# Kernel tuning notes

Measured on AMD Instinct MI355X. Metric: run time of the kernel, lower is better.

## Reference

```python
import jax, jax.numpy as jnp
import numpy as np

EMBED = 1024
HEADS = 16
HEAD_DIM = EMBED // HEADS
OUT = 1024


def setup_inputs() -> dict:
    key = jax.random.key(0)
    ks = jax.random.split(key, 6)
    x = jax.random.normal(ks[0], (4, 2048, EMBED), dtype=jnp.float32)
    # per-head projection weights, torch Linear convention: [out_features, in_features]
    s = 1.0 / np.sqrt(HEAD_DIM)
    Wv = jax.random.uniform(ks[1], (HEAD_DIM, HEAD_DIM), jnp.float32, -s, s)
    Wk = jax.random.uniform(ks[2], (HEAD_DIM, HEAD_DIM), jnp.float32, -s, s)
    Wq = jax.random.uniform(ks[3], (HEAD_DIM, HEAD_DIM), jnp.float32, -s, s)
    so = 1.0 / np.sqrt(EMBED)
    Wo = jax.random.uniform(ks[4], (OUT, EMBED), jnp.float32, -so, so)
    bo = jax.random.uniform(ks[5], (OUT,), jnp.float32, -so, so)
    return {"x": x, "Wq": Wq, "Wk": Wk, "Wv": Wv, "Wo": Wo, "bo": bo}


def reference(x, Wq, Wk, Wv, Wo, bo):
    N, L, _ = x.shape
    xh = x.reshape(N, L, HEADS, HEAD_DIM)  # nqhd
    q = jnp.einsum('nqhd,ed->nqhe', xh, Wq)
    k = jnp.einsum('nkhd,ed->nkhe', xh, Wk)
    v = jnp.einsum('nkhd,ed->nkhe', xh, Wv)
    # full score matrix [N, H, Q, K], scaled by sqrt(embed_size) as in source
    energy = jnp.einsum('nqhd,nkhd->nhqk', q, k) / np.sqrt(EMBED).astype(np.float32)
    attn = jax.nn.softmax(energy, axis=3)
    out = jnp.einsum('nhqk,nkhd->nqhd', attn, v).reshape(N, L, EMBED)
    return out @ Wo.T + bo
```

## Files before the change

### kernel.cpp

```cpp
#include <hip/hip_runtime.h>
#include <hip/hip_bf16.h>
#include <stdint.h>
#include <stddef.h>


typedef __attribute__((ext_vector_type(8))) short bf16x8;
typedef __attribute__((ext_vector_type(4))) float f32x4;
typedef __attribute__((ext_vector_type(4))) short short4v;
typedef __attribute__((ext_vector_type(2))) uint32_t uint2v;

__device__ __forceinline__ f32x4 mfma16(bf16x8 a, bf16x8 b, f32x4 c) {
    return __builtin_amdgcn_mfma_f32_16x16x32_bf16(a, b, c, 0, 0, 0);
}

__device__ __forceinline__ short f2bf(float x) {
    union { float f; uint32_t u; } v; v.f = x;
    uint32_t r = (v.u + 0x7FFFu + ((v.u >> 16) & 1u)) >> 16;
    return (short)(uint16_t)r;
}

__device__ __forceinline__ uint32_t pk2bf(float a, float b) {
    union { __hip_bfloat162 h; uint32_t u; } v;
    v.h = __float22bfloat162_rn(float2{a, b});
    return v.u;
}

__device__ __forceinline__ bf16x8 cvt8(const float* __restrict__ p) {
    f32x4 a = *(const f32x4*)p;
    f32x4 b = *(const f32x4*)(p + 4);
    bf16x8 r;
    r[0] = f2bf(a[0]); r[1] = f2bf(a[1]); r[2] = f2bf(a[2]); r[3] = f2bf(a[3]);
    r[4] = f2bf(b[0]); r[5] = f2bf(b[1]); r[6] = f2bf(b[2]); r[7] = f2bf(b[3]);
    return r;
}

__device__ __forceinline__ void swap16(uint32_t a, uint32_t b,
                                       uint32_t& lo, uint32_t& hi) {
#if __has_builtin(__builtin_amdgcn_permlane16_swap)
    uint2v r = __builtin_amdgcn_permlane16_swap(a, b, false, false);
    lo = r[0]; hi = r[1];
#else
    int lane = (int)(threadIdx.x & 63);
    uint32_t bl = (uint32_t)__shfl((int)b, lane & 47);
    uint32_t ah = (uint32_t)__shfl((int)a, lane | 16);
    lo = (lane & 16) ? bl : a;
    hi = (lane & 16) ? b : ah;
#endif
}

__global__ __launch_bounds__(256)
void wpack_kernel(const float* __restrict__ Wo, const float* __restrict__ Wq,
                  const float* __restrict__ Wk, const float* __restrict__ Wv,
                  short* __restrict__ wo_f, short* __restrict__ wqkv_f) {
    int b = blockIdx.x;
    if (b < 512) {
        int idx = b * 256 + threadIdx.x;
        int nrow = idx >> 7;
        int k0 = (idx & 127) * 8;
        bf16x8 v = cvt8(Wo + (size_t)nrow * 1024 + k0);
        int ntile = nrow >> 4, lcn = nrow & 15;
        int kseg = k0 >> 5, qd = (k0 >> 3) & 3;
        *(bf16x8*)(wo_f + ((size_t)(ntile * 32 + kseg) * 64 + qd * 16 + lcn) * 8) = v;
    } else {
        const float* W = (b == 512) ? Wq : (b == 513) ? Wk : Wv;
        short* dst = wqkv_f + (size_t)(b - 512) * 4096;
        for (int u = threadIdx.x; u < 512; u += 256) {
            int seg = u >> 6, ln = u & 63;
            int nt = seg >> 1, kf = seg & 1, lq = ln >> 4, lcn = ln & 15;
            bf16x8 v = cvt8(W + (nt * 16 + lcn) * 64 + kf * 32 + lq * 8);
            *(bf16x8*)(dst + u * 8) = v;
        }
    }
}

__global__ __launch_bounds__(256)
void kvproj_kernel(const float* __restrict__ x, const short* __restrict__ wqkv_f,
                   short* __restrict__ kf_ws, short* __restrict__ vf_ws) {
    __shared__ alignas(16) short kbuf[128 * 72];
    __shared__ alignas(16) short vbuf[64 * 136];
    int tid = threadIdx.x;
    int lt = blockIdx.x & 15, nh = blockIdx.x >> 4;
    int n = nh >> 4, h = nh & 15;
    int l0 = lt * 128, kt0 = lt * 2;
    int wv = tid >> 6, lane = tid & 63, quad = lane >> 4, lc = lane & 15;
    const short* wkf = wqkv_f + 4096 + lane * 8;
    const short* wvf = wqkv_f + 8192 + lane * 8;

    for (int u = tid; u < 1024; u += 256) {
        int r = u >> 3, c = (u & 7) * 8;
        *(bf16x8*)(kbuf + r * 72 + c) =
            cvt8(x + (size_t)(n * 2048 + l0 + r) * 1024 + h * 64 + c);
    }
    __syncthreads();

    bf16x8 xa[2][2];
    for (int mt = 0; mt < 2; ++mt)
        for (int kf = 0; kf < 2; ++kf)
            xa[mt][kf] = *(bf16x8*)(kbuf + (wv * 32 + mt * 16 + lc) * 72 + kf * 32 + quad * 8);

    f32x4 ka[2][4] = {}, va[2][4] = {};
    for (int nt = 0; nt < 4; ++nt)
        for (int kf = 0; kf < 2; ++kf) {
            bf16x8 wkb = *(const bf16x8*)(wkf + (nt * 2 + kf) * 512);
            bf16x8 wvb = *(const bf16x8*)(wvf + (nt * 2 + kf) * 512);
            for (int mt = 0; mt < 2; ++mt) {
                ka[mt][nt] = mfma16(xa[mt][kf], wkb, ka[mt][nt]);
                va[mt][nt] = mfma16(xa[mt][kf], wvb, va[mt][nt]);
            }
        }

    for (int mt = 0; mt < 2; ++mt) {
        int off = wv * 32 + mt * 16;
        for (int nt = 0; nt < 4; ++nt) {
            short4v pv;
            for (int i = 0; i < 4; ++i) {
                kbuf[(off + quad * 4 + i) * 72 + nt * 16 + lc] = f2bf(ka[mt][nt][i]);
                pv[i] = f2bf(va[mt][nt][i]);
            }
            *(short4v*)(vbuf + (nt * 16 + lc) * 136 + off + quad * 4) = pv;
        }
    }
    __syncthreads();

    size_t base = (size_t)nh * 131072 + (size_t)kt0 * 4096;
    for (int u = tid; u < 1024; u += 256) {
        int tile = u >> 9, rem = u & 511, seg = rem >> 6, ln = u & 63;
        int t = seg >> 1, kf = seg & 1;
        int lq = ln >> 4, ll = ln & 15;
        int bq = ((lq & 1) << 1) | (lq >> 1);
        bf16x8 kw = *(bf16x8*)(kbuf + (tile * 64 + t * 16 + ll) * 72 + kf * 32 + lq * 8);
        *(bf16x8*)(kf_ws + base + (size_t)tile * 4096 + seg * 512 + ln * 8) = kw;
        bf16x8 vw = *(bf16x8*)(vbuf + (t * 16 + ll) * 136 + tile * 64 + kf * 32 + bq * 8);
        *(bf16x8*)(vf_ws + base + (size_t)tile * 4096 + seg * 512 + ln * 8) = vw;
    }
}

__global__ __launch_bounds__(256, 2)
void flash_kernel(const float* __restrict__ x, const short* __restrict__ wqkv_f,
                  const short* __restrict__ kf_ws, const short* __restrict__ vf_ws,
                  short* __restrict__ ao) {
    __shared__ alignas(16) short pbuf[128 * 72];
    int tid = threadIdx.x;
    int nh = blockIdx.x & 63, qt = blockIdx.x >> 6;
    int n = nh >> 4, h = nh & 15;
    int q0 = qt * 128;
    int wv = tid >> 6, lane = tid & 63, quad = lane >> 4, lc = lane & 15;

    for (int u = tid; u < 1024; u += 256) {
        int r = u >> 3, c = (u & 7) * 8;
        *(bf16x8*)(pbuf + r * 72 + c) =
            cvt8(x + (size_t)(n * 2048 + q0 + r) * 1024 + h * 64 + c);
    }
    __syncthreads();
    {
        const short* wqf = wqkv_f + lane * 8;
        bf16x8 xa[2][2];
        for (int mt = 0; mt < 2; ++mt)
            for (int kf = 0; kf < 2; ++kf)
                xa[mt][kf] = *(bf16x8*)(pbuf + (wv * 32 + mt * 16 + lc) * 72 +
                                        kf * 32 + quad * 8);
        f32x4 qacc[2][4] = {};
        for (int nt = 0; nt < 4; ++nt)
            for (int kf = 0; kf < 2; ++kf) {
                bf16x8 wb = *(const bf16x8*)(wqf + (nt * 2 + kf) * 512);
                for (int mt = 0; mt < 2; ++mt)
                    qacc[mt][nt] = mfma16(xa[mt][kf], wb, qacc[mt][nt]);
            }
        const float QS = 0.04508422002778011f;
        for (int mt = 0; mt < 2; ++mt)
            for (int nt = 0; nt < 4; ++nt)
                for (int i = 0; i < 4; ++i)
                    pbuf[(wv * 32 + mt * 16 + quad * 4 + i) * 72 + nt * 16 + lc] =
                        f2bf(qacc[mt][nt][i] * QS);
    }
    __syncthreads();
    bf16x8 qa[2][2];
    for (int mt = 0; mt < 2; ++mt)
        for (int kf = 0; kf < 2; ++kf)
            qa[mt][kf] = *(bf16x8*)(pbuf + (wv * 32 + mt * 16 + lc) * 72 +
                                    kf * 32 + quad * 8);

    f32x4 o[2][4] = {};
    float lsum[2] = {0.f, 0.f};
    const short* kbase = kf_ws + (size_t)nh * 131072 + lane * 8;
    const short* vbase = vf_ws + (size_t)nh * 131072 + lane * 8;

    bf16x8 kN[4][2];
    bf16x8 vA[4][2];
    f32x4 s[2][4];

#pragma unroll
    for (int t = 0; t < 4; ++t)
        for (int kf = 0; kf < 2; ++kf)
            kN[t][kf] = *(const bf16x8*)(kbase + (t * 2 + kf) * 512);
#pragma unroll
    for (int q2 = 0; q2 < 2; ++q2)
        for (int t = 0; t < 4; ++t) {
            f32x4 acc = {};
            acc = mfma16(kN[t][0], qa[q2][0], acc);
            acc = mfma16(kN[t][1], qa[q2][1], acc);
            s[q2][t] = acc;
        }

    for (int kt = 0; kt < 32; ++kt) {
        const short* vp = vbase + (size_t)kt * 4096;
        const short* kp = kbase + (size_t)((kt + 1) & 31) * 4096;
#pragma unroll
        for (int t = 0; t < 4; ++t)
            for (int kf = 0; kf < 2; ++kf)
                vA[t][kf] = *(const bf16x8*)(vp + (t * 2 + kf) * 512);
#pragma unroll
        for (int t = 0; t < 4; ++t)
            for (int kf = 0; kf < 2; ++kf)
                kN[t][kf] = *(const bf16x8*)(kp + (t * 2 + kf) * 512);

#pragma unroll
        for (int q2 = 0; q2 < 2; ++q2) {
            uint32_t p0[4], p1[4];
            float ts = 0.f;
#pragma unroll
            for (int t = 0; t < 4; ++t) {
                float e0 = __builtin_amdgcn_exp2f(s[q2][t][0]);
                float e1 = __builtin_amdgcn_exp2f(s[q2][t][1]);
                float e2 = __builtin_amdgcn_exp2f(s[q2][t][2]);
                float e3 = __builtin_amdgcn_exp2f(s[q2][t][3]);
                ts += (e0 + e1) + (e2 + e3);
                p0[t] = pk2bf(e0, e1);
                p1[t] = pk2bf(e2, e3);
            }
            lsum[q2] += ts;
#pragma unroll
            for (int kf = 0; kf < 2; ++kf) {
                uint32_t r0, r1, r2, r3;
                swap16(p0[2 * kf], p0[2 * kf + 1], r0, r2);
                swap16(p1[2 * kf], p1[2 * kf + 1], r1, r3);
                union { uint32_t u[4]; bf16x8 v; } fr;
                fr.u[0] = r0; fr.u[1] = r1; fr.u[2] = r2; fr.u[3] = r3;
#pragma unroll
                for (int dt = 0; dt < 4; ++dt)
                    o[q2][dt] = mfma16(vA[dt][kf], fr.v, o[q2][dt]);
            }
        }

#pragma unroll
        for (int q2 = 0; q2 < 2; ++q2)
            for (int t = 0; t < 4; ++t) {
                f32x4 acc = {};
                acc = mfma16(kN[t][0], qa[q2][0], acc);
                acc = mfma16(kN[t][1], qa[q2][1], acc);
                s[q2][t] = acc;
            }
    }

    for (int q2 = 0; q2 < 2; ++q2) {
        float t = lsum[q2];
        t += __shfl_xor(t, 16, 64);
        t += __shfl_xor(t, 32, 64);
        float inv = 1.f / t;
        int mtile = (n * 2048 + q0) / 16 + wv * 2 + q2;
        for (int dt = 0; dt < 4; ++dt) {
            int kseg = h * 2 + (dt >> 1);
            int qd8 = ((dt & 1) * 4 + quad) >> 1;
            short4v pk;
            for (int i = 0; i < 4; ++i) pk[i] = f2bf(o[q2][dt][i] * inv);
            *(short4v*)(ao + (size_t)(mtile * 32 + kseg) * 512 +
                        (qd8 * 16 + lc) * 8 + (quad & 1) * 4) = pk;
        }
    }
}

__global__ __launch_bounds__(256)
void outgemm_kernel(const short* __restrict__ afb, const short* __restrict__ wfb,
                    const float* __restrict__ bo, float* __restrict__ out) {
    int tid = threadIdx.x;
    int bm = blockIdx.x & 63, bn = blockIdx.x >> 6;
    int m0 = bm * 128, n0 = bn * 128;
    int wv = tid >> 6, lane = tid & 63, quad = lane >> 4, lc = lane & 15;
    int wr = wv >> 1, wc = wv & 1;
    int mtb = bm * 8 + wr * 4;
    int ntb = bn * 8 + wc * 4;

    const short* ab = afb + lane * 8;
    const short* bb = wfb + lane * 8;

    f32x4 acc[4][4] = {};
    for (int kt = 0; kt < 32; ++kt) {
        bf16x8 af[4], bfr[4];
#pragma unroll
        for (int mt = 0; mt < 4; ++mt)
            af[mt] = *(const bf16x8*)(ab + ((size_t)(mtb + mt) * 32 + kt) * 512);
#pragma unroll
        for (int nt = 0; nt < 4; ++nt)
            bfr[nt] = *(const bf16x8*)(bb + ((size_t)(ntb + nt) * 32 + kt) * 512);
#pragma unroll
        for (int mt = 0; mt < 4; ++mt)
            for (int nt = 0; nt < 4; ++nt)
                acc[mt][nt] = mfma16(af[mt], bfr[nt], acc[mt][nt]);
    }
    for (int nt = 0; nt < 4; ++nt) {
        float bv = bo[n0 + wc * 64 + nt * 16 + lc];
        for (int mt = 0; mt < 4; ++mt)
            for (int i = 0; i < 4; ++i) {
                int m = m0 + wr * 64 + mt * 16 + quad * 4 + i;
                int nn = n0 + wc * 64 + nt * 16 + lc;
                out[(size_t)m * 1024 + nn] = acc[mt][nt][i] + bv;
            }
    }
}

extern "C" void kernel_launch(void* const* d_in, const int* in_sizes, int n_in,
                              void* d_out, int out_size, void* d_ws, size_t ws_size,
                              hipStream_t stream) {
    const float* x  = (const float*)d_in[0];
    const float* Wq = (const float*)d_in[1];
    const float* Wk = (const float*)d_in[2];
    const float* Wv = (const float*)d_in[3];
    const float* Wo = (const float*)d_in[4];
    const float* bo = (const float*)d_in[5];
    float* out = (float*)d_out;

    short* kf_ws   = (short*)d_ws;
    short* vf_ws   = kf_ws + 8388608;
    short* ao_ws   = vf_ws + 8388608;
    short* wo_f    = ao_ws + 8388608;
    short* wqkv_f  = wo_f + 1048576;

    wpack_kernel<<<dim3(515), dim3(256), 0, stream>>>(Wo, Wq, Wk, Wv, wo_f, wqkv_f);
    kvproj_kernel<<<dim3(1024), dim3(256), 0, stream>>>(x, wqkv_f, kf_ws, vf_ws);
    flash_kernel<<<dim3(1024), dim3(256), 0, stream>>>(x, wqkv_f, kf_ws, vf_ws, ao_ws);
    outgemm_kernel<<<dim3(512), dim3(256), 0, stream>>>(ao_ws, wo_f, bo, out);
}
```

Before: 233.3 us.

## Stage K/V tiles into double-buffered LDS via global_load_lds, shared across waves

```diff
diff --git a/kernel.cpp b/kernel.cpp
--- a/kernel.cpp
+++ b/kernel.cpp
@@ -32,6 +32,12 @@
     r[0] = f2bf(a[0]); r[1] = f2bf(a[1]); r[2] = f2bf(a[2]); r[3] = f2bf(a[3]);
     r[4] = f2bf(b[0]); r[5] = f2bf(b[1]); r[6] = f2bf(b[2]); r[7] = f2bf(b[3]);
     return r;
+}
+
+__device__ __forceinline__ void gl_lds16(const short* g, short* l) {
+    __builtin_amdgcn_global_load_lds(
+        (const __attribute__((address_space(1))) void*)g,
+        (__attribute__((address_space(3))) void*)l, 16, 0, 0);
 }
 
 __device__ __forceinline__ void swap16(uint32_t a, uint32_t b,
@@ -135,17 +141,18 @@
     }
 }
 
-__global__ __launch_bounds__(256, 2)
+__global__ __launch_bounds__(256, 4)
 void flash_kernel(const float* __restrict__ x, const short* __restrict__ wqkv_f,
                   const short* __restrict__ kf_ws, const short* __restrict__ vf_ws,
                   short* __restrict__ ao) {
-    __shared__ alignas(16) short pbuf[128 * 72];
+    __shared__ alignas(16) short lds[16384];
     int tid = threadIdx.x;
     int nh = blockIdx.x & 63, qt = blockIdx.x >> 6;
     int n = nh >> 4, h = nh & 15;
     int q0 = qt * 128;
     int wv = tid >> 6, lane = tid & 63, quad = lane >> 4, lc = lane & 15;
 
+    short* pbuf = lds;
     for (int u = tid; u < 1024; u += 256) {
         int r = u >> 3, c = (u & 7) * 8;
         *(bf16x8*)(pbuf + r * 72 + c) =
@@ -179,41 +186,57 @@
         for (int kf = 0; kf < 2; ++kf)
             qa[mt][kf] = *(bf16x8*)(pbuf + (wv * 32 + mt * 16 + lc) * 72 +
                                     kf * 32 + quad * 8);
+    __syncthreads();
+
+    const short* kbase = kf_ws + (size_t)nh * 131072 + lane * 8;
+    const short* vbase = vf_ws + (size_t)nh * 131072 + lane * 8;
+
+#pragma unroll
+    for (int i = 0; i < 4; ++i) {
+        int seg = wv * 4 + i;
+        const short* src = (seg < 8) ? (kbase + seg * 512)
+                                     : (vbase + (seg - 8) * 512);
+        gl_lds16(src, lds + seg * 512);
+    }
+    __syncthreads();
 
     f32x4 o[2][4] = {};
     float lsum[2] = {0.f, 0.f};
-    const short* kbase = kf_ws + (size_t)nh * 131072 + lane * 8;
-    const short* vbase = vf_ws + (size_t)nh * 131072 + lane * 8;
-
-    bf16x8 kN[4][2];
-    bf16x8 vA[4][2];
-    f32x4 s[2][4];
-
-#pragma unroll
-    for (int t = 0; t < 4; ++t)
-        for (int kf = 0; kf < 2; ++kf)
-            kN[t][kf] = *(const bf16x8*)(kbase + (t * 2 + kf) * 512);
-#pragma unroll
-    for (int q2 = 0; q2 < 2; ++q2)
-        for (int t = 0; t < 4; ++t) {
-            f32x4 acc = {};
-            acc = mfma16(kN[t][0], qa[q2][0], acc);
-            acc = mfma16(kN[t][1], qa[q2][1], acc);
-            s[q2][t] = acc;
-        }
 
     for (int kt = 0; kt < 32; ++kt) {
-        const short* vp = vbase + (size_t)kt * 4096;
-        const short* kp = kbase + (size_t)((kt + 1) & 31) * 4096;
+        int cur = kt & 1;
+        const short* lb = lds + cur * 8192;
+        {
+            int nkt = (kt + 1) & 31;
+            short* db = lds + (cur ^ 1) * 8192;
+#pragma unroll
+            for (int i = 0; i < 4; ++i) {
+                int seg = wv * 4 + i;
+                const short* src = (seg < 8)
+                    ? (kbase + (size_t)nkt * 4096 + seg * 512)
+                    : (vbase + (size_t)nkt * 4096 + (seg - 8) * 512);
+                gl_lds16(src, db + seg * 512);
+            }
+        }
+        bf16x8 kA[4][2];
 #pragma unroll
         for (int t = 0; t < 4; ++t)
             for (int kf = 0; kf < 2; ++kf)
-                vA[t][kf] = *(const bf16x8*)(vp + (t * 2 + kf) * 512);
+                kA[t][kf] = *(const bf16x8*)(lb + (t * 2 + kf) * 512 + lane * 8);
+        f32x4 s[2][4];
+#pragma unroll
+        for (int q2 = 0; q2 < 2; ++q2)
+            for (int t = 0; t < 4; ++t) {
+                f32x4 acc = {};
+                acc = mfma16(kA[t][0], qa[q2][0], acc);
+                acc = mfma16(kA[t][1], qa[q2][1], acc);
+                s[q2][t] = acc;
+            }
+        bf16x8 vA[4][2];
 #pragma unroll
         for (int t = 0; t < 4; ++t)
             for (int kf = 0; kf < 2; ++kf)
-                kN[t][kf] = *(const bf16x8*)(kp + (t * 2 + kf) * 512);
-
+                vA[t][kf] = *(const bf16x8*)(lb + 4096 + (t * 2 + kf) * 512 + lane * 8);
 #pragma unroll
         for (int q2 = 0; q2 < 2; ++q2) {
             uint32_t p0[4], p1[4];
@@ -241,15 +264,7 @@
                     o[q2][dt] = mfma16(vA[dt][kf], fr.v, o[q2][dt]);
             }
         }
-
-#pragma unroll
-        for (int q2 = 0; q2 < 2; ++q2)
-            for (int t = 0; t < 4; ++t) {
-                f32x4 acc = {};
-                acc = mfma16(kN[t][0], qa[q2][0], acc);
-                acc = mfma16(kN[t][1], qa[q2][1], acc);
-                s[q2][t] = acc;
-            }
+        __syncthreads();
     }
 
     for (int q2 = 0; q2 < 2; ++q2) {
```

Result: faster. 208.3 us (-10.7%).
